# Kernel tuning notes

Measured on AMD Instinct MI355X. Metric: run time of the kernel, lower is better.

## Reference

```python
import jax, jax.numpy as jnp
import numpy as np

B, C_HID, H, W = 2, 30, 1024, 1024
PS, PAD = 16, 4            # patch_size, patch_padding
MID, OUT = 80, 1
POST = 8                   # post_conv_layers
H_ERR, W_ERR = H // PS, W // PS
K_PER_B = int(H_ERR * W_ERR * 0.125)   # sampling top-k per batch = 512
P = B * K_PER_B
C_IN = C_HID + 1           # conv0 input channels = 31
KWIN = PS + 2 * PAD        # 24 = patch window incl. padding
N_PRE = PAD - 1            # conv1..conv3 (conv0 separate)
EPS = 1e-5


def _bn_params(key, c):
    k1, k2, k3, k4 = jax.random.split(key, 4)
    g = 1.0 + 0.1 * jax.random.normal(k1, (c,), jnp.float32)
    b = 0.1 * jax.random.normal(k2, (c,), jnp.float32)
    m = 0.1 * jax.random.normal(k3, (c,), jnp.float32)
    v = jax.random.uniform(k4, (c,), jnp.float32, 0.5, 1.5)
    return jnp.stack([g, b, m, v])  # (4, c)


def setup_inputs() -> dict:
    key = jax.random.key(0)
    ks = jax.random.split(key, 12)
    cw = lambda k, co, ci: 0.05 * jax.random.normal(k, (co, ci, 3, 3), jnp.float32)
    return {
        "pha": jax.random.normal(ks[0], (B, 1, H, W), jnp.float32),
        "err": jax.random.uniform(ks[1], (B, 1, H_ERR, W_ERR), jnp.float32),
        "hid": jax.random.normal(ks[2], (B, C_HID, H, W), jnp.float32),
        "w0": cw(ks[3], MID, C_IN),
        "bn0": _bn_params(ks[4], MID),
        "w_pre": 0.05 * jax.random.normal(ks[5], (N_PRE, MID, MID, 3, 3), jnp.float32),
        "bn_pre": jnp.stack([_bn_params(k, MID) for k in jax.random.split(ks[6], N_PRE)]),
        "w_post": 0.05 * jax.random.normal(ks[7], (POST - 1, MID, MID, 3, 3), jnp.float32),
        "bn_post": jnp.stack([_bn_params(k, MID) for k in jax.random.split(ks[8], POST - 1)]),
        "w_last": cw(ks[9], OUT, MID),
    }


def _conv(x, w, padding):
    return jax.lax.conv_general_dilated(x, w, (1, 1), padding,
        dimension_numbers=("NCHW", "OIHW", "NCHW"))


def _bn(x, p):  # eval-mode BatchNorm, p = (4, C)
    g, b, m, v = p
    inv = g * jax.lax.rsqrt(v + EPS)
    return x * inv[None, :, None, None] + (b - m * inv)[None, :, None, None]


def reference(pha, err, hid, w0, bn0, w_pre, bn_pre, w_post, bn_post, w_last):
    # --- select_refinement_regions (mode='sampling') ---
    err_flat = err.reshape(B, -1)                                   # (B, H_ERR*W_ERR)
    _, top_idx = jax.lax.top_k(err_flat, K_PER_B)                   # (B, K)
    ref = jnp.zeros_like(err_flat).at[jnp.arange(B)[:, None], top_idx].set(1.0)
    ref = ref * (err_flat > 0).astype(ref.dtype)                    # prevent_oversampling
    ref = ref.reshape(B, 1, H_ERR, W_ERR)
    # static-size nonzero: err>0 a.s. so exactly K per batch are selected
    b_idx = jnp.repeat(jnp.arange(B), K_PER_B)                      # (P,)
    flat = top_idx.reshape(-1)
    i_idx = flat // W_ERR
    j_idx = flat % W_ERR
    # --- crop_patch (unfold) on detached cat([hid, pha]) ---
    x = jax.lax.stop_gradient(jnp.concatenate([hid, pha], axis=1))  # (B, 31, H, W)
    xp = jnp.pad(x, ((0, 0), (0, 0), (PAD, PAD), (PAD, PAD)))
    rows = i_idx[:, None] * PS + jnp.arange(KWIN)[None, :]          # (P, 24)
    cols = j_idx[:, None] * PS + jnp.arange(KWIN)[None, :]
    patches = xp[b_idx[:, None, None], :, rows[:, :, None], cols[:, None, :]]  # (P,24,24,31)
    y = patches.transpose(0, 3, 1, 2)                               # (P, 31, 24, 24)
    # --- pre convs: valid 3x3, each shrinks by 2 (24 -> 16) ---
    y = jax.nn.relu(_bn(_conv(y, w0, "VALID"), bn0))
    for l in range(N_PRE):
        y = jax.nn.relu(_bn(_conv(y, w_pre[l], "VALID"), bn_pre[l]))
    # --- post convs: residual same-padded, last maps to out_channel ---
    for l in range(POST - 1):
        y = y + jax.nn.relu(_bn(_conv(y, w_post[l], "SAME"), bn_post[l]))
    y = _conv(y, w_last, "SAME")                                    # (P, 1, 16, 16)
    # --- replace_patch (scatter_nd) ---
    pha6 = pha.reshape(B, 1, H_ERR, PS, W_ERR, PS).transpose(0, 2, 4, 1, 3, 5)
    pha6 = pha6.at[b_idx, i_idx, j_idx].set(y)
    pha_out = pha6.transpose(0, 3, 1, 4, 2, 5).reshape(B, 1, H, W)
    return pha_out, ref
```

## Files before the change

### kernel.cpp

```cpp
#include <hip/hip_runtime.h>
#include <hip/hip_bf16.h>
#include <stdint.h>

typedef __hip_bfloat16 bf16;
typedef __attribute__((ext_vector_type(8))) short short8;
typedef __attribute__((ext_vector_type(4))) float f32x4;

__device__ __forceinline__ bf16 f2b(float x) { return __float2bfloat16(x); }

#define NW 8

#define A0_OFF 0
#define X_OFF  77440
#define A1_OFF 77440
#define A2_OFF 0
#define Z_OFF  57024
#define BB_OFF 114048
#define BS_OFF 147840
#define YF_OFF 0
#define SMEM_SZ 163200

__device__ __forceinline__ void gload_lds16(const void* g, char* l) {
    __builtin_amdgcn_global_load_lds(
        (const __attribute__((address_space(1))) unsigned int*)g,
        (__attribute__((address_space(3))) unsigned int*)l, 16, 0, 0);
}

__global__ __launch_bounds__(1024) void topk_kernel(const float* __restrict__ err,
                                                    float* __restrict__ ref_out,
                                                    int* __restrict__ sel)
{
    __shared__ uint64_t keys[4096];
    const int b = blockIdx.x >> 4, slice = blockIdx.x & 15;
    const float* e = err + b * 4096;
    for (int t = threadIdx.x; t < 4096; t += 1024) {
        uint32_t u = __float_as_uint(e[t]);
        u ^= (u >> 31) ? 0xFFFFFFFFu : 0x80000000u;
        keys[t] = ((uint64_t)u << 32) | (uint32_t)(4095 - t);
    }
    __syncthreads();
    const int cand = slice * 256 + (threadIdx.x >> 2);
    const int part = threadIdx.x & 3;
    const uint64_t mykey = keys[cand];
    int r = 0;
#pragma unroll 8
    for (int j = part * 1024; j < part * 1024 + 1024; ++j)
        r += (keys[j] > mykey) ? 1 : 0;
    r += __shfl_xor(r, 1);
    r += __shfl_xor(r, 2);
    if (part == 0) {
        bool s = (r < 512);
        if (s) sel[b * 512 + r] = cand;
        ref_out[b * 4096 + cand] = (s && e[cand] > 0.f) ? 1.f : 0.f;
    }
}

__global__ void wt_kernel(const float* __restrict__ w0, const float* __restrict__ wpre,
                          const float* __restrict__ wpost, const float* __restrict__ w_last,
                          const float* __restrict__ bn0, const float* __restrict__ bn_pre,
                          const float* __restrict__ bn_post,
                          bf16* __restrict__ Wf, float* __restrict__ wlastT,
                          float* __restrict__ bnbeta)
{
    int t = blockIdx.x * blockDim.x + threadIdx.x;
    if (t < 714240) {
        int l, tap, kb, rem;
        if (t < 23040) { l = 0; tap = t / 2560; kb = 0; rem = t % 2560; }
        else {
            int t2 = t - 23040;
            l = 1 + t2 / 69120;
            int r0 = t2 % 69120;
            tap = r0 / 7680;
            int r1 = r0 % 7680;
            kb = r1 / 2560; rem = r1 % 2560;
        }
        int n = rem / 512, r2 = rem % 512, lane = r2 / 8, i = r2 % 8;
        int co = n * 16 + (lane & 15);
        int k  = kb * 32 + (lane >> 4) * 8 + i;
        float v = 0.f;
        if (l == 0)      { if (k < 31) v = w0[(co * 31 + k) * 9 + tap]; }
        else if (l <= 3) { if (k < 80) v = wpre[(((l - 1) * 80 + co) * 80 + k) * 9 + tap]; }
        else             { if (k < 80) v = wpost[(((l - 4) * 80 + co) * 80 + k) * 9 + tap]; }
        const float* src = (l == 0) ? bn0 : (l <= 3 ? bn_pre + (l - 1) * 320
                                                    : bn_post + (l - 4) * 320);
        float inv = src[co] * rsqrtf(src[240 + co] + 1e-5f);
        Wf[t] = f2b(v * inv);
    } else if (t < 714960) {
        int i = t - 714240; int tap = i / 80, ci = i % 80;
        wlastT[tap * 80 + ci] = w_last[ci * 9 + tap];
    } else if (t < 715840) {
        int i = t - 714960; int l = i / 80, co = i % 80;
        const float* src = (l == 0) ? bn0 : (l <= 3 ? bn_pre + (l - 1) * 320
                                                    : bn_post + (l - 4) * 320);
        float inv = src[co] * rsqrtf(src[240 + co] + 1e-5f);
        bnbeta[i] = src[80 + co] - src[160 + co] * inv;
    }
}

__global__ void copy_kernel(const uint4* __restrict__ src, uint4* __restrict__ dst, int n)
{
    int t = blockIdx.x * blockDim.x + threadIdx.x;
    if (t < n) dst[t] = src[t];
}

template <int NIN, int NOUT, int KB, int ISTR, int OSTR>
__device__ __forceinline__ void conv_small(char* sm, int inBase, int outBase,
                                           const char* __restrict__ Wl,
                                           const float* __restrict__ bnl)
{
    const int tid = threadIdx.x;
    const int wv = tid >> 6, lane = tid & 63;
    const int r = lane & 15, kg = lane >> 4;
    constexpr int NPIX = NOUT * NOUT;
    constexpr int NMT = (NPIX + 15) / 16;
    constexpr int NSTEP = 9 * KB;

    int aA[2][2];
    bool act[2][2];
#pragma unroll
    for (int pp = 0; pp < 2; ++pp)
#pragma unroll
        for (int mm = 0; mm < 2; ++mm) {
            int mt = (wv + pp * NW) * 2 + mm;
            int pix = mt * 16 + r;
            act[pp][mm] = (mt < NMT);
            int cp = pix < NPIX ? pix : NPIX - 1;
            aA[pp][mm] = inBase + ((cp / NOUT) * NIN + cp % NOUT) * ISTR + kg * 16;
        }

    float betb[5];
#pragma unroll
    for (int n = 0; n < 5; ++n) betb[n] = bnl[n * 16 + r];
    asm volatile("" :: "v"(betb[0]), "v"(betb[1]), "v"(betb[2]),
                       "v"(betb[3]), "v"(betb[4]));

    f32x4 acc[2][2][5];
#pragma unroll
    for (int pp = 0; pp < 2; ++pp)
#pragma unroll
        for (int mm = 0; mm < 2; ++mm)
#pragma unroll
            for (int n = 0; n < 5; ++n) {
                f32x4 bi = {betb[n], betb[n], betb[n], betb[n]};
                acc[pp][mm][n] = bi;
            }

    auto stage = [&](int step) {
        if (tid < 320)
            gload_lds16(Wl + step * 5120 + tid * 16,
                        sm + BS_OFF + (step % 3) * 5120 + tid * 16);
    };

    asm volatile("s_waitcnt vmcnt(0)" ::: "memory");
    stage(0); stage(1);
    asm volatile("s_waitcnt vmcnt(1) lgkmcnt(0)" ::: "memory");
    __builtin_amdgcn_s_barrier();

#pragma unroll
    for (int s = 0; s < NSTEP; ++s) {
        if (s + 2 < NSTEP) stage(s + 2);
        const int tap = s / KB, kb = s % KB;
        const int dtap = (tap / 3) * NIN + (tap % 3);
        const int sb = BS_OFF + (s % 3) * 5120;
        short8 bf[5];
#pragma unroll
        for (int n = 0; n < 5; ++n)
            bf[n] = *(const short8*)(sm + sb + n * 1024 + lane * 16);
#pragma unroll
        for (int pp = 0; pp < 2; ++pp)
#pragma unroll
            for (int mm = 0; mm < 2; ++mm) {
                if (!act[pp][mm]) continue;
                short8 af = *(const short8*)(sm + aA[pp][mm] + dtap * ISTR + kb * 64);
#pragma unroll
                for (int n = 0; n < 5; ++n)
                    acc[pp][mm][n] = __builtin_amdgcn_mfma_f32_16x16x32_bf16(
                        af, bf[n], acc[pp][mm][n], 0, 0, 0);
            }
        if (s + 2 < NSTEP)
            asm volatile("s_waitcnt vmcnt(1) lgkmcnt(0)" ::: "memory");
        else
            asm volatile("s_waitcnt vmcnt(0) lgkmcnt(0)" ::: "memory");
        __builtin_amdgcn_s_barrier();
    }

#pragma unroll
    for (int pp = 0; pp < 2; ++pp)
#pragma unroll
        for (int mm = 0; mm < 2; ++mm) {
            int mt = (wv + pp * NW) * 2 + mm;
            if (mt < NMT) {
#pragma unroll
                for (int n = 0; n < 5; ++n) {
                    int co = n * 16 + r;
#pragma unroll
                    for (int j = 0; j < 4; ++j) {
                        int pix = mt * 16 + kg * 4 + j;
                        if (pix < NPIX) {
                            float o = fmaxf(acc[pp][mm][n][j], 0.f);
                            *(bf16*)(sm + outBase + pix * OSTR + co * 2) = f2b(o);
                        }
                    }
                }
            }
        }
}

template <int MODE, int STOREZ>
__device__ __forceinline__ void conv_big(char* sm, int inBase,
                                         const char* __restrict__ Wl,
                                         const float* __restrict__ bnl,
                                         f32x4 (&Yreg)[2][5])
{
    const int tid = threadIdx.x;
    const int wv = tid >> 6, lane = tid & 63;
    const int r = lane & 15, kg = lane >> 4;

    float betb[5];
#pragma unroll
    for (int n = 0; n < 5; ++n) betb[n] = bnl[n * 16 + r];
    asm volatile("" :: "v"(betb[0]), "v"(betb[1]), "v"(betb[2]),
                       "v"(betb[3]), "v"(betb[4]));

    f32x4 acc[2][5];
#pragma unroll
    for (int mm = 0; mm < 2; ++mm)
#pragma unroll
        for (int n = 0; n < 5; ++n) {
            f32x4 bi = {betb[n], betb[n], betb[n], betb[n]};
            acc[mm][n] = bi;
        }

    int aBase[2];
#pragma unroll
    for (int mm = 0; mm < 2; ++mm) {
        int mt = 2 * wv + mm;
        aBase[mm] = inBase + (mt * 18 + r) * 176 + kg * 16;
    }

    auto stage = [&](int step) {
        const char* src = Wl + step * 15360;
        char* dst = sm + BB_OFF + (step % 3) * 16384;
        gload_lds16(src + tid * 16, dst + tid * 16);
        gload_lds16(src + 8192 + tid * 16, dst + 8192 + tid * 16);
    };

    asm volatile("s_waitcnt vmcnt(0)" ::: "memory");
    stage(0); stage(1);
    asm volatile("s_waitcnt vmcnt(2) lgkmcnt(0)" ::: "memory");
    __builtin_amdgcn_s_barrier();

#pragma unroll
    for (int s = 0; s < 9; ++s) {
        if (s + 2 < 9) stage(s + 2);
        const int dt = ((s / 3) * 18 + (s % 3)) * 176;
        const int sb = BB_OFF + (s % 3) * 16384;
#pragma unroll
        for (int kb = 0; kb < 3; ++kb) {
            short8 bf[5];
#pragma unroll
            for (int n = 0; n < 5; ++n)
                bf[n] = *(const short8*)(sm + sb + kb * 5120 + n * 1024 + lane * 16);
#pragma unroll
            for (int mm = 0; mm < 2; ++mm) {
                short8 af = *(const short8*)(sm + aBase[mm] + dt + kb * 64);
#pragma unroll
                for (int n = 0; n < 5; ++n)
                    acc[mm][n] = __builtin_amdgcn_mfma_f32_16x16x32_bf16(
                        af, bf[n], acc[mm][n], 0, 0, 0);
            }
        }
        if (s + 2 < 9)
            asm volatile("s_waitcnt vmcnt(2) lgkmcnt(0)" ::: "memory");
        else
            asm volatile("s_waitcnt vmcnt(0) lgkmcnt(0)" ::: "memory");
        __builtin_amdgcn_s_barrier();
    }

#pragma unroll
    for (int mm = 0; mm < 2; ++mm) {
        int y = 2 * wv + mm;
#pragma unroll
        for (int n = 0; n < 5; ++n) {
            int co = n * 16 + r;
#pragma unroll
            for (int j = 0; j < 4; ++j) {
                int x = kg * 4 + j;
                float o = fmaxf(acc[mm][n][j], 0.f);
                if (MODE == 1) {
                    Yreg[mm][n][j] = o;
                    *(bf16*)(sm + Z_OFF + ((y + 1) * 18 + x + 1) * 176 + co * 2) = f2b(o);
                } else {
                    float nv = Yreg[mm][n][j] + o;
                    Yreg[mm][n][j] = nv;
                    if (STOREZ)
                        *(bf16*)(sm + Z_OFF + ((y + 1) * 18 + x + 1) * 176 + co * 2) = f2b(nv);
                }
            }
        }
    }
}

__global__ __launch_bounds__(512, 2) void refine_kernel(
    const int* __restrict__ sel,
    const float* __restrict__ hid, const float* __restrict__ pha,
    const char* __restrict__ Wf, const float* __restrict__ wlastT,
    const float* __restrict__ bnbeta, float* __restrict__ out)
{
    __shared__ __align__(16) char sm[SMEM_SZ];
    const int tid = threadIdx.x;
    const int p = blockIdx.x;
    const int e = sel[p];
    const int b = p >> 9;
    const int pi = e >> 6, pj = e & 63;

    {
        uint4 z4 = {0u, 0u, 0u, 0u};
        uint4* z = (uint4*)sm;
        for (int t = tid; t < SMEM_SZ / 16; t += 512) z[t] = z4;
    }
    __syncthreads();

    const int r0 = pi * 16 - 4, c0 = pj * 16 - 4;
    for (int t = tid; t < 32 * 576; t += 512) {
        int c = t / 576, pix = t - c * 576;
        int gr = r0 + pix / 24, gc = c0 + pix % 24;
        float v = 0.f;
        if (c < 31 && (unsigned)gr < 1024u && (unsigned)gc < 1024u)
            v = (c < 30) ? hid[((b * 30 + c) * 1024 + gr) * 1024 + gc]
                         : pha[(b * 1024 + gr) * 1024 + gc];
        *(bf16*)(sm + X_OFF + pix * 80 + c * 2) = f2b(v);
    }

    conv_small<24, 22, 1,  80, 160>(sm, X_OFF,  A0_OFF, Wf,          bnbeta);
    conv_small<22, 20, 3, 160, 176>(sm, A0_OFF, A1_OFF, Wf + 46080,  bnbeta + 80);
    conv_small<20, 18, 3, 176, 176>(sm, A1_OFF, A2_OFF, Wf + 184320, bnbeta + 160);

    for (int t = tid; t < 68 * 11; t += 512) {
        int cell = t / 11, part = t % 11;
        int i, j;
        if (cell < 18)      { i = 0;  j = cell; }
        else if (cell < 36) { i = 17; j = cell - 18; }
        else { int k = cell - 36; i = 1 + (k >> 1); j = (k & 1) ? 17 : 0; }
        *(uint4*)(sm + Z_OFF + (i * 18 + j) * 176 + part * 16) = (uint4){0u, 0u, 0u, 0u};
    }

    f32x4 Yreg[2][5];
    conv_big<1, 1>(sm, A2_OFF, Wf + 322560, bnbeta + 240, Yreg);
#pragma unroll 1
    for (int l = 0; l < 6; ++l)
        conv_big<2, 1>(sm, Z_OFF, Wf + 460800 + l * 138240, bnbeta + 320 + l * 80, Yreg);
    conv_big<2, 0>(sm, Z_OFF, Wf + 460800 + 6 * 138240, bnbeta + 800, Yreg);

    {
        const int wv = tid >> 6, lane = tid & 63;
        const int r = lane & 15, kg = lane >> 4;
#pragma unroll
        for (int mm = 0; mm < 2; ++mm) {
            int mt = 2 * wv + mm;
#pragma unroll
            for (int n = 0; n < 5; ++n) {
                int co = n * 16 + r;
#pragma unroll
                for (int j = 0; j < 4; ++j) {
                    int pix = mt * 16 + kg * 4 + j;
                    *(float*)(sm + YF_OFF + pix * 336 + co * 4) = Yreg[mm][n][j];
                }
            }
        }
    }
    __syncthreads();

    {
        int pix = tid >> 1, half = tid & 1;
        int y = pix >> 4, x = pix & 15;
        float accv = 0.f;
        const float* Yb = (const float*)(sm + YF_OFF);
#pragma unroll
        for (int tap = 0; tap < 9; ++tap) {
            int iy = y + tap / 3 - 1, ix = x + tap % 3 - 1;
            if ((unsigned)iy >= 16u || (unsigned)ix >= 16u) continue;
            const float* yp = Yb + (iy * 16 + ix) * 84;
            const float* wp = wlastT + tap * 80;
            for (int c = half * 40; c < half * 40 + 40; c += 4) {
                float4 a  = *(const float4*)(yp + c);
                float4 w4 = *(const float4*)(wp + c);
                accv += a.x * w4.x + a.y * w4.y + a.z * w4.z + a.w * w4.w;
            }
        }
        accv += __shfl_xor(accv, 1);
        if (half == 0)
            out[b * 1048576 + (pi * 16 + y) * 1024 + pj * 16 + x] = accv;
    }
}

extern "C" void kernel_launch(void* const* d_in, const int* in_sizes, int n_in,
                              void* d_out, int out_size, void* d_ws, size_t ws_size,
                              hipStream_t stream)
{
    (void)in_sizes; (void)n_in; (void)out_size; (void)ws_size;
    const float* pha     = (const float*)d_in[0];
    const float* err     = (const float*)d_in[1];
    const float* hid     = (const float*)d_in[2];
    const float* w0      = (const float*)d_in[3];
    const float* bn0     = (const float*)d_in[4];
    const float* w_pre   = (const float*)d_in[5];
    const float* bn_pre  = (const float*)d_in[6];
    const float* w_post  = (const float*)d_in[7];
    const float* bn_post = (const float*)d_in[8];
    const float* w_last  = (const float*)d_in[9];
    float* out = (float*)d_out;

    char* ws = (char*)d_ws;
    bf16*  Wf     = (bf16*)ws;
    float* wlastT = (float*)(ws + 1429504);
    float* bnbeta = (float*)(ws + 1432384);
    int*   sel    = (int*)(ws + 1441792);

    hipLaunchKernelGGL(wt_kernel, dim3(2797), dim3(256), 0, stream,
                       w0, w_pre, w_post, w_last, bn0, bn_pre, bn_post,
                       Wf, wlastT, bnbeta);
    hipLaunchKernelGGL(topk_kernel, dim3(32), dim3(1024), 0, stream,
                       err, out + 2097152, sel);
    hipLaunchKernelGGL(copy_kernel, dim3(2048), dim3(256), 0, stream,
                       (const uint4*)pha, (uint4*)out, 524288);
    hipLaunchKernelGGL(refine_kernel, dim3(1024), dim3(512), 0, stream,
                       sel, hid, pha, (const char*)Wf, wlastT, bnbeta, out);
}
```

Before: 491.7 us.

## Restage conv weights: register double-buffer for pre convs, coarse LDS stages for post

The pre convs now read their bf16 weight fragments straight from global memory into a register double buffer instead of staging them through LDS with a barrier per step. The post convs get a reordered weight layout (kb-major across all 9 taps), so each LDS stage holds a whole 46 KB k-slice. Those stages are double-buffered with one barrier per k-slice rather than one per tap. The goal is fewer workgroup barriers and wait stalls in the MFMA loops. The cost is duplicated global/L2 weight traffic per wave in the pre convs, more LDS taken by the larger stages, and higher register pressure.

Result: faster. 479.1 us (-2.6%).

```diff
diff --git a/kernel.cpp b/kernel.cpp
--- a/kernel.cpp
+++ b/kernel.cpp
@@ -7,16 +7,15 @@
 typedef __attribute__((ext_vector_type(4))) float f32x4;
 
 __device__ __forceinline__ bf16 f2b(float x) { return __float2bfloat16(x); }
-
-#define NW 8
 
 #define A0_OFF 0
 #define X_OFF  77440
 #define A1_OFF 77440
 #define A2_OFF 0
 #define Z_OFF  57024
-#define BB_OFF 114048
-#define BS_OFF 147840
+#define S0_OFF 0
+#define S1_OFF 114048
+#define PB_OFF 160128
 #define YF_OFF 0
 #define SMEM_SZ 163200
 
@@ -70,9 +69,15 @@
             int t2 = t - 23040;
             l = 1 + t2 / 69120;
             int r0 = t2 % 69120;
-            tap = r0 / 7680;
-            int r1 = r0 % 7680;
-            kb = r1 / 2560; rem = r1 % 2560;
+            if (l <= 3) {
+                tap = r0 / 7680;
+                int r1 = r0 % 7680;
+                kb = r1 / 2560; rem = r1 % 2560;
+            } else {
+                kb = r0 / 23040;
+                int r1 = r0 % 23040;
+                tap = r1 / 2560; rem = r1 % 2560;
+            }
         }
         int n = rem / 512, r2 = rem % 512, lane = r2 / 8, i = r2 % 8;
         int co = n * 16 + (lane & 15);
@@ -103,25 +108,41 @@
     if (t < n) dst[t] = src[t];
 }
 
-template <int NIN, int NOUT, int KB, int ISTR, int OSTR>
-__device__ __forceinline__ void conv_small(char* sm, int inBase, int outBase,
-                                           const char* __restrict__ Wl,
-                                           const float* __restrict__ bnl)
+template <int NIN, int NOUT, int KB, int ISTR, int OSTR, int MODE, int BORDER>
+__device__ __forceinline__ void conv_reg(char* sm, int inBase, int outBase,
+                                         const char* __restrict__ Wl,
+                                         const float* __restrict__ bnl,
+                                         f32x4 (&Yreg)[2][5])
 {
     const int tid = threadIdx.x;
     const int wv = tid >> 6, lane = tid & 63;
     const int r = lane & 15, kg = lane >> 4;
-    constexpr int NPIX = NOUT * NOUT;
-    constexpr int NMT = (NPIX + 15) / 16;
+    constexpr int NPIX  = NOUT * NOUT;
+    constexpr int NMT   = (NPIX + 15) / 16;
     constexpr int NSTEP = 9 * KB;
-
-    int aA[2][2];
-    bool act[2][2];
-#pragma unroll
-    for (int pp = 0; pp < 2; ++pp)
+    constexpr int PMAX  = (NMT > 16) ? 2 : 1;
+
+    asm volatile("s_waitcnt lgkmcnt(0)" ::: "memory");
+    __builtin_amdgcn_s_barrier();
+
+    if (BORDER) {
+        for (int t = tid; t < 68 * 11; t += 512) {
+            int cell = t / 11, part = t % 11;
+            int i, j;
+            if (cell < 18)      { i = 0;  j = cell; }
+            else if (cell < 36) { i = 17; j = cell - 18; }
+            else { int k = cell - 36; i = 1 + (k >> 1); j = (k & 1) ? 17 : 0; }
+            *(uint4*)(sm + Z_OFF + (i * 18 + j) * 176 + part * 16) = (uint4){0u, 0u, 0u, 0u};
+        }
+    }
+
+    int aA[PMAX][2];
+    bool act[PMAX][2];
+#pragma unroll
+    for (int pp = 0; pp < PMAX; ++pp)
 #pragma unroll
         for (int mm = 0; mm < 2; ++mm) {
-            int mt = (wv + pp * NW) * 2 + mm;
+            int mt = (wv + pp * 8) * 2 + mm;
             int pix = mt * 16 + r;
             act[pp][mm] = (mt < NMT);
             int cp = pix < NPIX ? pix : NPIX - 1;
@@ -131,12 +152,10 @@
     float betb[5];
 #pragma unroll
     for (int n = 0; n < 5; ++n) betb[n] = bnl[n * 16 + r];
-    asm volatile("" :: "v"(betb[0]), "v"(betb[1]), "v"(betb[2]),
-                       "v"(betb[3]), "v"(betb[4]));
-
-    f32x4 acc[2][2][5];
-#pragma unroll
-    for (int pp = 0; pp < 2; ++pp)
+
+    f32x4 acc[PMAX][2][5];
+#pragma unroll
+    for (int pp = 0; pp < PMAX; ++pp)
 #pragma unroll
         for (int mm = 0; mm < 2; ++mm)
 #pragma unroll
@@ -145,29 +164,21 @@
                 acc[pp][mm][n] = bi;
             }
 
-    auto stage = [&](int step) {
-        if (tid < 320)
-            gload_lds16(Wl + step * 5120 + tid * 16,
-                        sm + BS_OFF + (step % 3) * 5120 + tid * 16);
-    };
-
-    asm volatile("s_waitcnt vmcnt(0)" ::: "memory");
-    stage(0); stage(1);
-    asm volatile("s_waitcnt vmcnt(1) lgkmcnt(0)" ::: "memory");
-    __builtin_amdgcn_s_barrier();
-
-#pragma unroll
-    for (int s = 0; s < NSTEP; ++s) {
-        if (s + 2 < NSTEP) stage(s + 2);
+    short8 B0[5], B1[5];
+#pragma unroll
+    for (int n = 0; n < 5; ++n)
+        B0[n] = *(const short8*)(Wl + n * 1024 + lane * 16);
+
+    auto body = [&](short8 (&Bc)[5], short8 (&Bn)[5], int s) {
+        if (s + 1 < NSTEP) {
+#pragma unroll
+            for (int n = 0; n < 5; ++n)
+                Bn[n] = *(const short8*)(Wl + (s + 1) * 5120 + n * 1024 + lane * 16);
+        }
         const int tap = s / KB, kb = s % KB;
         const int dtap = (tap / 3) * NIN + (tap % 3);
-        const int sb = BS_OFF + (s % 3) * 5120;
-        short8 bf[5];
-#pragma unroll
-        for (int n = 0; n < 5; ++n)
-            bf[n] = *(const short8*)(sm + sb + n * 1024 + lane * 16);
-#pragma unroll
-        for (int pp = 0; pp < 2; ++pp)
+#pragma unroll
+        for (int pp = 0; pp < PMAX; ++pp)
 #pragma unroll
             for (int mm = 0; mm < 2; ++mm) {
                 if (!act[pp][mm]) continue;
@@ -175,21 +186,22 @@
 #pragma unroll
                 for (int n = 0; n < 5; ++n)
                     acc[pp][mm][n] = __builtin_amdgcn_mfma_f32_16x16x32_bf16(
-                        af, bf[n], acc[pp][mm][n], 0, 0, 0);
-            }
-        if (s + 2 < NSTEP)
-            asm volatile("s_waitcnt vmcnt(1) lgkmcnt(0)" ::: "memory");
-        else
-            asm volatile("s_waitcnt vmcnt(0) lgkmcnt(0)" ::: "memory");
-        __builtin_amdgcn_s_barrier();
-    }
-
-#pragma unroll
-    for (int pp = 0; pp < 2; ++pp)
+                        af, Bc[n], acc[pp][mm][n], 0, 0, 0);
+            }
+    };
+
+#pragma unroll
+    for (int s2 = 0; s2 < NSTEP; s2 += 2) {
+        body(B0, B1, s2);
+        if (s2 + 1 < NSTEP) body(B1, B0, s2 + 1);
+    }
+
+#pragma unroll
+    for (int pp = 0; pp < PMAX; ++pp)
 #pragma unroll
         for (int mm = 0; mm < 2; ++mm) {
-            int mt = (wv + pp * NW) * 2 + mm;
-            if (mt < NMT) {
+            int mt = (wv + pp * 8) * 2 + mm;
+            if (act[pp][mm]) {
 #pragma unroll
                 for (int n = 0; n < 5; ++n) {
                     int co = n * 16 + r;
@@ -198,7 +210,13 @@
                         int pix = mt * 16 + kg * 4 + j;
                         if (pix < NPIX) {
                             float o = fmaxf(acc[pp][mm][n][j], 0.f);
-                            *(bf16*)(sm + outBase + pix * OSTR + co * 2) = f2b(o);
+                            if (MODE == 0) {
+                                *(bf16*)(sm + outBase + pix * OSTR + co * 2) = f2b(o);
+                            } else {
+                                Yreg[mm][n][j] = o;
+                                int y = pix >> 4, x = pix & 15;
+                                *(bf16*)(sm + Z_OFF + ((y + 1) * 18 + x + 1) * 176 + co * 2) = f2b(o);
+                            }
                         }
                     }
                 }
@@ -206,99 +224,15 @@
         }
 }
 
-template <int MODE, int STOREZ>
-__device__ __forceinline__ void conv_big(char* sm, int inBase,
-                                         const char* __restrict__ Wl,
-                                         const float* __restrict__ bnl,
-                                         f32x4 (&Yreg)[2][5])
-{
-    const int tid = threadIdx.x;
-    const int wv = tid >> 6, lane = tid & 63;
-    const int r = lane & 15, kg = lane >> 4;
-
-    float betb[5];
-#pragma unroll
-    for (int n = 0; n < 5; ++n) betb[n] = bnl[n * 16 + r];
-    asm volatile("" :: "v"(betb[0]), "v"(betb[1]), "v"(betb[2]),
-                       "v"(betb[3]), "v"(betb[4]));
-
-    f32x4 acc[2][5];
-#pragma unroll
-    for (int mm = 0; mm < 2; ++mm)
-#pragma unroll
-        for (int n = 0; n < 5; ++n) {
-            f32x4 bi = {betb[n], betb[n], betb[n], betb[n]};
-            acc[mm][n] = bi;
-        }
-
-    int aBase[2];
-#pragma unroll
-    for (int mm = 0; mm < 2; ++mm) {
-        int mt = 2 * wv + mm;
-        aBase[mm] = inBase + (mt * 18 + r) * 176 + kg * 16;
-    }
-
-    auto stage = [&](int step) {
-        const char* src = Wl + step * 15360;
-        char* dst = sm + BB_OFF + (step % 3) * 16384;
-        gload_lds16(src + tid * 16, dst + tid * 16);
-        gload_lds16(src + 8192 + tid * 16, dst + 8192 + tid * 16);
-    };
-
-    asm volatile("s_waitcnt vmcnt(0)" ::: "memory");
-    stage(0); stage(1);
-    asm volatile("s_waitcnt vmcnt(2) lgkmcnt(0)" ::: "memory");
-    __builtin_amdgcn_s_barrier();
-
-#pragma unroll
-    for (int s = 0; s < 9; ++s) {
-        if (s + 2 < 9) stage(s + 2);
-        const int dt = ((s / 3) * 18 + (s % 3)) * 176;
-        const int sb = BB_OFF + (s % 3) * 16384;
-#pragma unroll
-        for (int kb = 0; kb < 3; ++kb) {
-            short8 bf[5];
-#pragma unroll
-            for (int n = 0; n < 5; ++n)
-                bf[n] = *(const short8*)(sm + sb + kb * 5120 + n * 1024 + lane * 16);
-#pragma unroll
-            for (int mm = 0; mm < 2; ++mm) {
-                short8 af = *(const short8*)(sm + aBase[mm] + dt + kb * 64);
-#pragma unroll
-                for (int n = 0; n < 5; ++n)
-                    acc[mm][n] = __builtin_amdgcn_mfma_f32_16x16x32_bf16(
-                        af, bf[n], acc[mm][n], 0, 0, 0);
-            }
-        }
-        if (s + 2 < 9)
-            asm volatile("s_waitcnt vmcnt(2) lgkmcnt(0)" ::: "memory");
-        else
-            asm volatile("s_waitcnt vmcnt(0) lgkmcnt(0)" ::: "memory");
-        __builtin_amdgcn_s_barrier();
-    }
-
-#pragma unroll
-    for (int mm = 0; mm < 2; ++mm) {
-        int y = 2 * wv + mm;
-#pragma unroll
-        for (int n = 0; n < 5; ++n) {
-            int co = n * 16 + r;
-#pragma unroll
-            for (int j = 0; j < 4; ++j) {
-                int x = kg * 4 + j;
-                float o = fmaxf(acc[mm][n][j], 0.f);
-                if (MODE == 1) {
-                    Yreg[mm][n][j] = o;
-                    *(bf16*)(sm + Z_OFF + ((y + 1) * 18 + x + 1) * 176 + co * 2) = f2b(o);
-                } else {
-                    float nv = Yreg[mm][n][j] + o;
-                    Yreg[mm][n][j] = nv;
-                    if (STOREZ)
-                        *(bf16*)(sm + Z_OFF + ((y + 1) * 18 + x + 1) * 176 + co * 2) = f2b(nv);
-                }
-            }
-        }
-    }
+__device__ __forceinline__ void post_stage(char* sm, const char* src, int slotOff, int tid)
+{
+    char* dst = sm + slotOff;
+    gload_lds16(src + tid * 16,         dst + tid * 16);
+    gload_lds16(src + 8192 + tid * 16,  dst + 8192 + tid * 16);
+    gload_lds16(src + 16384 + tid * 16, dst + 16384 + tid * 16);
+    gload_lds16(src + 24576 + tid * 16, dst + 24576 + tid * 16);
+    gload_lds16(src + 32768 + tid * 16, dst + 32768 + tid * 16);
+    gload_lds16(src + 37888 + tid * 16, dst + 37888 + tid * 16);
 }
 
 __global__ __launch_bounds__(512, 2) void refine_kernel(
@@ -331,27 +265,102 @@
                          : pha[(b * 1024 + gr) * 1024 + gc];
         *(bf16*)(sm + X_OFF + pix * 80 + c * 2) = f2b(v);
     }
-
-    conv_small<24, 22, 1,  80, 160>(sm, X_OFF,  A0_OFF, Wf,          bnbeta);
-    conv_small<22, 20, 3, 160, 176>(sm, A0_OFF, A1_OFF, Wf + 46080,  bnbeta + 80);
-    conv_small<20, 18, 3, 176, 176>(sm, A1_OFF, A2_OFF, Wf + 184320, bnbeta + 160);
-
-    for (int t = tid; t < 68 * 11; t += 512) {
-        int cell = t / 11, part = t % 11;
-        int i, j;
-        if (cell < 18)      { i = 0;  j = cell; }
-        else if (cell < 36) { i = 17; j = cell - 18; }
-        else { int k = cell - 36; i = 1 + (k >> 1); j = (k & 1) ? 17 : 0; }
-        *(uint4*)(sm + Z_OFF + (i * 18 + j) * 176 + part * 16) = (uint4){0u, 0u, 0u, 0u};
-    }
+    for (int t = tid; t < 560; t += 512)
+        ((float*)(sm + PB_OFF))[t] = bnbeta[320 + t];
 
     f32x4 Yreg[2][5];
-    conv_big<1, 1>(sm, A2_OFF, Wf + 322560, bnbeta + 240, Yreg);
+
+    conv_reg<24, 22, 1,  80, 160, 0, 0>(sm, X_OFF,  A0_OFF, Wf,           bnbeta,       Yreg);
+    conv_reg<22, 20, 3, 160, 176, 0, 0>(sm, A0_OFF, A1_OFF, Wf + 46080,   bnbeta + 80,  Yreg);
+    conv_reg<20, 18, 3, 176, 176, 0, 0>(sm, A1_OFF, A2_OFF, Wf + 184320,  bnbeta + 160, Yreg);
+    conv_reg<18, 16, 3, 176, 176, 1, 1>(sm, A2_OFF, 0,      Wf + 322560,  bnbeta + 240, Yreg);
+
+    {
+        const int wv = tid >> 6, lane = tid & 63;
+        const int r = lane & 15, kg = lane >> 4;
+        const char* postW = Wf + 460800;
+        const float* ldsBeta = (const float*)(sm + PB_OFF);
+
+        int aBase[2];
+#pragma unroll
+        for (int mm = 0; mm < 2; ++mm)
+            aBase[mm] = Z_OFF + ((2 * wv + mm) * 18 + r) * 176 + kg * 16;
+
+        asm volatile("s_waitcnt lgkmcnt(0)" ::: "memory");
+        __builtin_amdgcn_s_barrier();
+        post_stage(sm, postW, S0_OFF, tid);
+        asm volatile("s_waitcnt vmcnt(0) lgkmcnt(0)" ::: "memory");
+        __builtin_amdgcn_s_barrier();
+
 #pragma unroll 1
-    for (int l = 0; l < 6; ++l)
-        conv_big<2, 1>(sm, Z_OFF, Wf + 460800 + l * 138240, bnbeta + 320 + l * 80, Yreg);
-    conv_big<2, 0>(sm, Z_OFF, Wf + 460800 + 6 * 138240, bnbeta + 800, Yreg);
-
+        for (int l = 0; l < 7; ++l) {
+            float betb[5];
+#pragma unroll
+            for (int n = 0; n < 5; ++n) betb[n] = ldsBeta[l * 80 + n * 16 + r];
+            f32x4 acc[2][5];
+#pragma unroll
+            for (int mm = 0; mm < 2; ++mm)
+#pragma unroll
+                for (int n = 0; n < 5; ++n) {
+                    f32x4 bi = {betb[n], betb[n], betb[n], betb[n]};
+                    acc[mm][n] = bi;
+                }
+
+#pragma unroll
+            for (int k = 0; k < 3; ++k) {
+                const int g = l * 3 + k;
+                if (g < 20)
+                    post_stage(sm, postW + (g + 1) * 46080,
+                               ((g + 1) & 1) ? S1_OFF : S0_OFF, tid);
+                const int slot = (g & 1) ? S1_OFF : S0_OFF;
+                const int aK0 = aBase[0] + k * 64, aK1 = aBase[1] + k * 64;
+#pragma unroll
+                for (int tap = 0; tap < 9; ++tap) {
+                    const int dt = ((tap / 3) * 18 + (tap % 3)) * 176;
+                    short8 bfv[5];
+#pragma unroll
+                    for (int n = 0; n < 5; ++n)
+                        bfv[n] = *(const short8*)(sm + slot + tap * 5120 + n * 1024 + lane * 16);
+                    short8 af0 = *(const short8*)(sm + aK0 + dt);
+                    short8 af1 = *(const short8*)(sm + aK1 + dt);
+#pragma unroll
+                    for (int n = 0; n < 5; ++n)
+                        acc[0][n] = __builtin_amdgcn_mfma_f32_16x16x32_bf16(
+                            af0, bfv[n], acc[0][n], 0, 0, 0);
+#pragma unroll
+                    for (int n = 0; n < 5; ++n)
+                        acc[1][n] = __builtin_amdgcn_mfma_f32_16x16x32_bf16(
+                            af1, bfv[n], acc[1][n], 0, 0, 0);
+                }
+                asm volatile("s_waitcnt vmcnt(0) lgkmcnt(0)" ::: "memory");
+                __builtin_amdgcn_s_barrier();
+            }
+
+#pragma unroll
+            for (int mm = 0; mm < 2; ++mm) {
+                int y = 2 * wv + mm;
+#pragma unroll
+                for (int n = 0; n < 5; ++n) {
+                    int co = n * 16 + r;
+#pragma unroll
+                    for (int j = 0; j < 4; ++j) {
+                        int x = kg * 4 + j;
+                        float o = fmaxf(acc[mm][n][j], 0.f);
+                        float nv = Yreg[mm][n][j] + o;
+                        Yreg[mm][n][j] = nv;
+                        if (l < 6)
+                            *(bf16*)(sm + Z_OFF + ((y + 1) * 18 + x + 1) * 176 + co * 2) = f2b(nv);
+                    }
+                }
+            }
+            if (l < 6) {
+                asm volatile("s_waitcnt lgkmcnt(0)" ::: "memory");
+                __builtin_amdgcn_s_barrier();
+            }
+        }
+    }
+
+    __syncthreads();
     {
         const int wv = tid >> 6, lane = tid & 63;
         const int r = lane & 15, kg = lane >> 4;
```
